# Performance work log

Hardware: AMD Instinct MI355X
Metric: run time of the kernel (lower is better)

Reference implementation:

```python
import math
import jax, jax.numpy as jnp
import numpy as np

EMBED = 512
HEADS = 2
HEAD_DIM = EMBED // HEADS


def setup_inputs() -> dict:
    key = jax.random.key(0)
    ks = jax.random.split(key, 10)
    s = 1.0 / math.sqrt(EMBED)
    return {
        "text_embeds": jax.random.normal(ks[0], (64, 32, EMBED), jnp.float32),
        "video_embeds": jax.random.normal(ks[1], (128, 64, EMBED), jnp.float32),
        "Wq": jax.random.normal(ks[2], (EMBED, EMBED), jnp.float32) * s,
        "bq": jnp.zeros((EMBED,), jnp.float32),
        "Wk": jax.random.normal(ks[3], (EMBED, EMBED), jnp.float32) * s,
        "bk": jnp.zeros((EMBED,), jnp.float32),
        "Wv": jax.random.normal(ks[4], (EMBED, EMBED), jnp.float32) * s,
        "bv": jnp.zeros((EMBED,), jnp.float32),
        "Wo": jax.random.normal(ks[5], (EMBED, EMBED), jnp.float32) * s,
        "bo": jnp.zeros((EMBED,), jnp.float32),
    }


def reference(text_embeds, video_embeds, Wq, bq, Wk, bk, Wv, bv, Wo, bo):
    num_texts, num_words, _ = text_embeds.shape
    num_vids, num_frames, _ = video_embeds.shape
    # projections (torch Linear: x @ W.T + b)
    q = (text_embeds @ Wq.T + bq).reshape(num_texts, num_words, HEADS, HEAD_DIM)
    k = (video_embeds @ Wk.T + bk).reshape(num_vids, num_frames, HEADS, HEAD_DIM)
    v = (video_embeds @ Wv.T + bv).reshape(num_vids, num_frames, HEADS, HEAD_DIM)
    # 5D cross attention logits: [vids, texts, heads, frames, words]
    logits = jnp.einsum('avhd,bthd->abhvt', k, q) / math.sqrt(HEAD_DIM)
    weights = jax.nn.softmax(logits, axis=3)  # softmax over frames
    attn = jnp.einsum('avhd,abhvt->abhtd', v, weights)  # [a,b,h,t,d]
    # faithful to torch: reshape (a,b,h,t,d) -> (a,b,t,h*d) in row-major order
    attn = attn.reshape(num_vids, num_texts, num_words, EMBED)
    attn = attn.mean(axis=0)  # [texts, words, embed]
    return attn @ Wo.T + bo
```

## Files before the change

kernel.cpp:

```cpp
#include <hip/hip_runtime.h>
#include <hip/hip_bf16.h>
#include <math.h>

#define EMBED  512
#define HEADS  2
#define HDIM   256
#define NTEXT  64
#define NWORD  32
#define NVID   128
#define NFRM   64

typedef __attribute__((ext_vector_type(8))) short      short8;
typedef __attribute__((ext_vector_type(8))) unsigned short ushort8;
typedef __attribute__((ext_vector_type(4))) float      float4v;
typedef __attribute__((ext_vector_type(4))) unsigned short ushort4v;

__device__ __forceinline__ unsigned short f2bf(float x) {
    __hip_bfloat16 h = __float2bfloat16(x);
    return *(unsigned short*)&h;
}
__device__ __forceinline__ float bf2f(unsigned short u) {
    __hip_bfloat16 h = *(__hip_bfloat16*)&u;
    return __bfloat162float(h);
}

__device__ __forceinline__ void gload_lds16(unsigned short* dst, const unsigned short* src) {
#if __has_builtin(__builtin_amdgcn_global_load_lds)
    __builtin_amdgcn_global_load_lds((const __attribute__((address_space(1))) void*)src,
                                     (__attribute__((address_space(3))) void*)dst,
                                     16, 0, 0);
#else
    *(ushort8*)dst = *(const ushort8*)src;
#endif
}

__global__ __launch_bounds__(256)
void cvt5(const float* __restrict__ s0, const float* __restrict__ s1,
          const float* __restrict__ s2, const float* __restrict__ s3,
          const float* __restrict__ s4, unsigned short* __restrict__ dst) {
    const int y = blockIdx.y;
    const float* s; size_t off; int n4;
    if (y == 0)      { s = s0; off = 0;       n4 = 262144;  }
    else if (y == 1) { s = s1; off = 1048576; n4 = 1048576; }
    else if (y == 2) { s = s2; off = 5242880; n4 = 65536;   }
    else if (y == 3) { s = s3; off = 5505024; n4 = 65536;   }
    else             { s = s4; off = 5767168; n4 = 65536;   }
    unsigned short* d = dst + off;
    for (int i = blockIdx.x * 256 + threadIdx.x; i < n4; i += 512 * 256) {
        float4v f = ((const float4v*)s)[i];
        ((ushort4v*)d)[i] = (ushort4v){f2bf(f.x), f2bf(f.y), f2bf(f.z), f2bf(f.w)};
    }
}

__global__ __launch_bounds__(256)
void proj_qkv(const unsigned short* __restrict__ text, const unsigned short* __restrict__ video,
              const unsigned short* __restrict__ Wqb, const float* __restrict__ bq,
              const unsigned short* __restrict__ Wkb, const float* __restrict__ bk,
              const unsigned short* __restrict__ Wvb, const float* __restrict__ bv,
              unsigned short* __restrict__ qout,
              unsigned short* __restrict__ Kgf, unsigned short* __restrict__ Vgf) {
    const int mb = blockIdx.x, nb = blockIdx.y;
    const int bj = nb * 128;
    const unsigned short *A, *W;
    const float* bias;
    int op, arow0, abase = 0;
    if (mb < 16)      { op = 0; A = text;  W = Wqb; bias = bq; arow0 = mb * 128; }
    else if (mb < 80) { op = 1; A = video; W = Wkb; bias = bk; abase = (mb - 16) * 2; arow0 = abase * 64; }
    else              { op = 2; A = video; W = Wvb; bias = bv; abase = (mb - 80) * 2; arow0 = abase * 64; }

    __shared__ __align__(16) unsigned char smem[65536];

    const int tid = threadIdx.x;
    const int w = tid >> 6, lane = tid & 63;
    const int lm = lane & 15, qd = lane >> 4;
    const int wr = w >> 1, wc = w & 1;

    float4v acc[4][4];
    #pragma unroll
    for (int rt = 0; rt < 4; ++rt)
        #pragma unroll
        for (int ct = 0; ct < 4; ++ct) acc[rt][ct] = (float4v){0.f, 0.f, 0.f, 0.f};

    auto STAGE = [&](int buf, int k0) {
        unsigned short* AbL = (unsigned short*)(smem + buf * 32768);
        unsigned short* WbL = (unsigned short*)(smem + buf * 32768 + 16384);
        #pragma unroll
        for (int it = 0; it < 4; ++it) {
            const int s = tid + it * 256;
            const int r = s >> 3, c8 = s & 7;
            const int sc = (c8 ^ (r & 7)) * 8;
            gload_lds16(&AbL[(size_t)s * 8], &A[(size_t)(arow0 + r) * 512 + k0 + sc]);
            gload_lds16(&WbL[(size_t)s * 8], &W[(size_t)(bj    + r) * 512 + k0 + sc]);
        }
    };

    STAGE(0, 0);
    __syncthreads();
    int cur = 0;
    for (int ks = 0; ks < 8; ++ks) {
        if (ks < 7) STAGE(cur ^ 1, (ks + 1) * 64);
        const unsigned short* AbL = (const unsigned short*)(smem + cur * 32768);
        const unsigned short* WbL = (const unsigned short*)(smem + cur * 32768 + 16384);
        #pragma unroll
        for (int kq = 0; kq < 2; ++kq) {
            const int scol = (kq * 32 + qd * 8) ^ ((lm & 7) * 8);
            short8 af[4], bf[4];
            #pragma unroll
            for (int rt = 0; rt < 4; ++rt)
                af[rt] = *(const short8*)&AbL[(wr * 64 + rt * 16 + lm) * 64 + scol];
            #pragma unroll
            for (int ct = 0; ct < 4; ++ct)
                bf[ct] = *(const short8*)&WbL[(wc * 64 + ct * 16 + lm) * 64 + scol];
            #pragma unroll
            for (int rt = 0; rt < 4; ++rt)
                #pragma unroll
                for (int ct = 0; ct < 4; ++ct)
                    acc[rt][ct] = __builtin_amdgcn_mfma_f32_16x16x32_bf16(af[rt], bf[ct], acc[rt][ct], 0, 0, 0);
        }
        __syncthreads();
        cur ^= 1;
    }

    if (op == 0) {
        #pragma unroll
        for (int rt = 0; rt < 4; ++rt)
            #pragma unroll
            for (int ct = 0; ct < 4; ++ct) {
                const int c = bj + wc * 64 + ct * 16 + lm;
                const float bb = bias[c];
                #pragma unroll
                for (int reg = 0; reg < 4; ++reg) {
                    const int r = arow0 + wr * 64 + rt * 16 + qd * 4 + reg;
                    qout[(size_t)r * 512 + c] = f2bf((acc[rt][ct][reg] + bb) * 0.0625f);
                }
            }
        return;
    }

    const int a   = abase + wr;
    const int bjs = bj + wc * 64;
    const int h      = bjs >> 8;
    const int bj_rel = bjs & 255;
    unsigned short (*Eb)[72] = (unsigned short (*)[72])(smem + w * 9216);
    const size_t base = ((size_t)(h * 128 + a)) * 16384;

    if (op == 1) {
        #pragma unroll
        for (int ct = 0; ct < 4; ++ct) {
            const int dl = ct * 16 + lm;
            const float bb = bias[bjs + dl];
            #pragma unroll
            for (int rt = 0; rt < 4; ++rt)
                #pragma unroll
                for (int reg = 0; reg < 4; ++reg)
                    Eb[rt * 16 + qd * 4 + reg][dl] = f2bf(acc[rt][ct][reg] + bb);
        }
        __syncthreads();
        #pragma unroll
        for (int it = 0; it < 8; ++it) {
            const int s = lane + it * 64;
            const int ntf = s >> 7, kqr = (s >> 6) & 1, l = s & 63;
            const int v = ntf * 16 + (l & 15);
            const int dl = kqr * 32 + (l >> 4) * 8;
            ushort8 val = *(const ushort8*)&Eb[v][dl];
            *(ushort8*)&Kgf[base + ((size_t)(ntf * 8 + (bj_rel >> 5) + kqr) * 64 + l) * 8] = val;
        }
    } else {
        #pragma unroll
        for (int ct = 0; ct < 4; ++ct) {
            const int dl = ct * 16 + lm;
            const float bb = bias[bjs + dl];
            #pragma unroll
            for (int rt = 0; rt < 4; ++rt)
                #pragma unroll
                for (int reg = 0; reg < 4; ++reg)
                    Eb[dl][rt * 16 + qd * 4 + reg] = f2bf(acc[rt][ct][reg] + bb);
        }
        __syncthreads();
        #pragma unroll
        for (int it = 0; it < 8; ++it) {
            const int s = lane + it * 64;
            const int ntr = s >> 7, kqv = (s >> 6) & 1, l = s & 63;
            const int dl = ntr * 16 + (l & 15);
            const int v0 = kqv * 32 + (l >> 4) * 8;
            ushort8 val = *(const ushort8*)&Eb[dl][v0];
            *(ushort8*)&Vgf[base + ((size_t)(((bj_rel >> 4) + ntr) * 2 + kqv) * 64 + l) * 8] = val;
        }
    }
}

__global__ __launch_bounds__(512, 2)
void attn9(const unsigned short* __restrict__ Kgf,
           const unsigned short* __restrict__ Vgf,
           const unsigned short* __restrict__ q,
           unsigned short* __restrict__ partg) {
    const int c  = blockIdx.x;
    const int h  = blockIdx.y;
    const int tg = blockIdx.z;
    const int tid = threadIdx.x;
    const int w = tid >> 6, lane = tid & 63;
    const int lm = lane & 15, qd = lane >> 4;
    const int wt = w >> 1;
    const int fh = w & 1;
    const int b = tg * 4 + wt;

    __shared__ __align__(16) unsigned short Kb[2][16384];
    __shared__ __align__(16) unsigned short Vb[2][16384];
    __shared__ __align__(16) unsigned short Pf[4][2][2][512];
    __shared__ __align__(16) float Ex[4][2][2][16][2];

    short8 qf[2][8];
    #pragma unroll
    for (int mt = 0; mt < 2; ++mt)
        #pragma unroll
        for (int kq = 0; kq < 8; ++kq)
            qf[mt][kq] = *(const short8*)
                &q[((size_t)(b * 32 + mt * 16 + lm)) * 512 + h * 256 + kq * 32 + qd * 8];

    float4v pacc[2][8];
    #pragma unroll
    for (int mt = 0; mt < 2; ++mt)
        #pragma unroll
        for (int nd = 0; nd < 8; ++nd) pacc[mt][nd] = (float4v){0.f, 0.f, 0.f, 0.f};

    const size_t vb0 = (size_t)(h * 128 + c * 16) * 16384;

    #pragma unroll
    for (int i = 0; i < 4; ++i) {
        const int s = tid + i * 512;
        gload_lds16(&Kb[0][(size_t)s * 8], &Kgf[vb0 + (size_t)s * 8]);
        gload_lds16(&Vb[0][(size_t)s * 8], &Vgf[vb0 + (size_t)s * 8]);
    }
    #pragma unroll
    for (int i = 0; i < 4; ++i) {
        const int s = tid + i * 512;
        gload_lds16(&Kb[1][(size_t)s * 8], &Kgf[vb0 + 16384 + (size_t)s * 8]);
        gload_lds16(&Vb[1][(size_t)s * 8], &Vgf[vb0 + 16384 + (size_t)s * 8]);
    }
    __syncthreads();

    for (int ai = 0; ai < 16; ++ai) {
        const int cur = ai & 1;

        float4v lacc[2][2];
        #pragma unroll
        for (int nt = 0; nt < 2; ++nt)
            #pragma unroll
            for (int mt = 0; mt < 2; ++mt) lacc[nt][mt] = (float4v){0.f, 0.f, 0.f, 0.f};
        #pragma unroll
        for (int kq = 0; kq < 8; ++kq) {
            #pragma unroll
            for (int nt = 0; nt < 2; ++nt) {
                const short8 kf = *(const short8*)
                    &Kb[cur][(((fh * 2 + nt) * 8 + kq) * 64 + lane) * 8];
                lacc[nt][0] = __builtin_amdgcn_mfma_f32_16x16x32_bf16(kf, qf[0][kq], lacc[nt][0], 0, 0, 0);
                lacc[nt][1] = __builtin_amdgcn_mfma_f32_16x16x32_bf16(kf, qf[1][kq], lacc[nt][1], 0, 0, 0);
            }
        }

        float m2[2], sv[2], e[2][2][4];
        #pragma unroll
        for (int mt = 0; mt < 2; ++mt) {
            float mm = lacc[0][mt][0];
            #pragma unroll
            for (int nt = 0; nt < 2; ++nt)
                #pragma unroll
                for (int r = 0; r < 4; ++r) mm = fmaxf(mm, lacc[nt][mt][r]);
            mm = fmaxf(mm, __shfl_xor(mm, 16));
            mm = fmaxf(mm, __shfl_xor(mm, 32));
            float ss = 0.f;
            #pragma unroll
            for (int nt = 0; nt < 2; ++nt)
                #pragma unroll
                for (int r = 0; r < 4; ++r) {
                    const float ev = __expf(lacc[nt][mt][r] - mm);
                    e[mt][nt][r] = ev;
                    ss += ev;
                }
            ss += __shfl_xor(ss, 16);
            ss += __shfl_xor(ss, 32);
            m2[mt] = mm; sv[mt] = ss;
            if (qd == 0) {
                Ex[wt][fh][mt][lm][0] = mm;
                Ex[wt][fh][mt][lm][1] = ss;
            }
        }
        __syncthreads();

        #pragma unroll
        for (int mt = 0; mt < 2; ++mt) {
            const float om = Ex[wt][fh ^ 1][mt][lm][0];
            const float os = Ex[wt][fh ^ 1][mt][lm][1];
            const float M   = fmaxf(m2[mt], om);
            const float den = sv[mt] * __expf(m2[mt] - M) + os * __expf(om - M);
            const float fac = __expf(m2[mt] - M) / den;
            #pragma unroll
            for (int nt = 0; nt < 2; ++nt) {
                ushort4v pv;
                pv.x = f2bf(e[mt][nt][0] * fac);
                pv.y = f2bf(e[mt][nt][1] * fac);
                pv.z = f2bf(e[mt][nt][2] * fac);
                pv.w = f2bf(e[mt][nt][3] * fac);
                *(ushort4v*)&Pf[wt][mt][fh][(lm + 16 * (nt * 2 + (qd >> 1))) * 8 + (qd & 1) * 4] = pv;
            }
        }
        __syncthreads();

        #pragma unroll
        for (int kqv = 0; kqv < 2; ++kqv) {
            const short8 pf0 = *(const short8*)&Pf[wt][0][kqv][lane * 8];
            const short8 pf1 = *(const short8*)&Pf[wt][1][kqv][lane * 8];
            #pragma unroll
            for (int nd = 0; nd < 8; ++nd) {
                const short8 vf = *(const short8*)
                    &Vb[cur][(((fh * 8 + nd) * 2 + kqv) * 64 + lane) * 8];
                pacc[0][nd] = __builtin_amdgcn_mfma_f32_16x16x32_bf16(pf0, vf, pacc[0][nd], 0, 0, 0);
                pacc[1][nd] = __builtin_amdgcn_mfma_f32_16x16x32_bf16(pf1, vf, pacc[1][nd], 0, 0, 0);
            }
        }
        __syncthreads();

        if (ai < 14) {
            const size_t kb = vb0 + (size_t)(ai + 2) * 16384;
            #pragma unroll
            for (int i = 0; i < 4; ++i) {
                const int s = tid + i * 512;
                gload_lds16(&Kb[cur][(size_t)s * 8], &Kgf[kb + (size_t)s * 8]);
                gload_lds16(&Vb[cur][(size_t)s * 8], &Vgf[kb + (size_t)s * 8]);
            }
        }
    }

    unsigned short* part = partg + (size_t)c * 1048576;
    #pragma unroll
    for (int mt = 0; mt < 2; ++mt)
        #pragma unroll
        for (int nd = 0; nd < 8; ++nd)
            #pragma unroll
            for (int r = 0; r < 4; ++r) {
                const int t = mt * 16 + qd * 4 + r;
                const int d = fh * 128 + nd * 16 + lm;
                const int row = b * 32 + h * 16 + (t >> 1);
                const int col = (t & 1) * 256 + d;
                part[(size_t)row * 512 + col] = f2bf(pacc[mt][nd][r]);
            }
}

__global__ __launch_bounds__(256)
void reduce8(unsigned short* __restrict__ partg) {
    const size_t i = ((size_t)blockIdx.x * 256 + threadIdx.x) * 8;
    float s[8];
    #pragma unroll
    for (int j = 0; j < 8; ++j) s[j] = 0.f;
    #pragma unroll
    for (int p = 0; p < 8; ++p) {
        ushort8 u = *(const ushort8*)&partg[(size_t)p * 1048576 + i];
        #pragma unroll
        for (int j = 0; j < 8; ++j) s[j] += bf2f(u[j]);
    }
    ushort8 o;
    #pragma unroll
    for (int j = 0; j < 8; ++j) o[j] = f2bf(s[j] * 0.0078125f);
    *(ushort8*)&partg[i] = o;
}

__global__ __launch_bounds__(256)
void proj_o(const unsigned short* __restrict__ Abf, const float* __restrict__ W,
            const float* __restrict__ bias, float* __restrict__ C) {
    __shared__ __align__(16) unsigned short Ab[64][72];
    __shared__ __align__(16) unsigned short Wb[64][72];
    const int tid = threadIdx.x;
    const int bi = blockIdx.x * 64, bj = blockIdx.y * 64;
    const int w = tid >> 6, lane = tid & 63;
    const int lm = lane & 15, qd = lane >> 4;

    float4v acc[4];
    #pragma unroll
    for (int nt = 0; nt < 4; ++nt) acc[nt] = (float4v){0.f, 0.f, 0.f, 0.f};

    for (int k0 = 0; k0 < 512; k0 += 64) {
        #pragma unroll
        for (int it = 0; it < 2; ++it) {
            const int s = tid + it * 256;
            const int r = s >> 3, c8 = (s & 7) * 8;
            *(ushort8*)&Ab[r][c8] = *(const ushort8*)&Abf[(size_t)(bi + r) * 512 + k0 + c8];
        }
        #pragma unroll
        for (int it = 0; it < 4; ++it) {
            const int s = tid + it * 256;
            const int r = s >> 4, c4 = (s & 15) * 4;
            float4v fw = *(const float4v*)&W[(size_t)(bj + r) * 512 + k0 + c4];
            *(ushort4v*)&Wb[r][c4] = (ushort4v){f2bf(fw.x), f2bf(fw.y), f2bf(fw.z), f2bf(fw.w)};
        }
        __syncthreads();
        #pragma unroll
        for (int kq = 0; kq < 2; ++kq) {
            const short8 af = *(const short8*)&Ab[w * 16 + lm][kq * 32 + qd * 8];
            #pragma unroll
            for (int nt = 0; nt < 4; ++nt) {
                const short8 bf = *(const short8*)&Wb[nt * 16 + lm][kq * 32 + qd * 8];
                acc[nt] = __builtin_amdgcn_mfma_f32_16x16x32_bf16(af, bf, acc[nt], 0, 0, 0);
            }
        }
        __syncthreads();
    }
    #pragma unroll
    for (int nt = 0; nt < 4; ++nt) {
        const int cc = bj + nt * 16 + lm;
        const float bb = bias[cc];
        #pragma unroll
        for (int reg = 0; reg < 4; ++reg) {
            const int r = bi + w * 16 + qd * 4 + reg;
            C[(size_t)r * 512 + cc] = acc[nt][reg] + bb;
        }
    }
}

extern "C" void kernel_launch(void* const* d_in, const int* in_sizes, int n_in,
                              void* d_out, int out_size, void* d_ws, size_t ws_size,
                              hipStream_t stream) {
    const float* text  = (const float*)d_in[0];
    const float* video = (const float*)d_in[1];
    const float* Wq = (const float*)d_in[2];
    const float* bq = (const float*)d_in[3];
    const float* Wk = (const float*)d_in[4];
    const float* bk = (const float*)d_in[5];
    const float* Wv = (const float*)d_in[6];
    const float* bv = (const float*)d_in[7];
    const float* Wo = (const float*)d_in[8];
    const float* bo = (const float*)d_in[9];

    unsigned short* Kgf   = (unsigned short*)d_ws;
    unsigned short* Vgf   = (unsigned short*)((char*)d_ws + (8u << 20));
    unsigned short* partg = (unsigned short*)((char*)d_ws + (16u << 20));
    unsigned short* textbf  = partg;
    unsigned short* videobf = partg + 1048576;
    unsigned short* wqbf    = partg + 5242880;
    unsigned short* wkbf    = partg + 5505024;
    unsigned short* wvbf    = partg + 5767168;
    unsigned short* qbf   = (unsigned short*)d_out;
    float*          out   = (float*)d_out;

    cvt5<<<dim3(512, 5), 256, 0, stream>>>(text, video, Wq, Wk, Wv, partg);
    proj_qkv<<<dim3(144, 4), 256, 0, stream>>>(textbf, videobf, wqbf, bq, wkbf, bk,
                                               wvbf, bv, qbf, Kgf, Vgf);
    attn9<<<dim3(8, 2, 16), 512, 0, stream>>>(Kgf, Vgf, qbf, partg);
    reduce8<<<dim3(512), 256, 0, stream>>>(partg);
    proj_o<<<dim3(32, 8), 256, 0, stream>>>(partg, Wo, bo, out);
}
```

Baseline: 167.1 us.

## Fuse fp32-to-bf16 conversion into QKV projection and partial reduction into output projection

Removes the separate conversion kernel by loading fp32 inputs and weights straight into registers in the QKV projection, converting to bf16 and writing to LDS with register-staged double buffering. Also folds the eight-way partial-sum reduction into the output projection, which now uses 256-column tiles so each block reduces its A rows only once. The intent is fewer launches and less intermediate global traffic. The cost is higher register pressure, loss of the async direct-to-LDS loads, and only 64 blocks in the output projection.

Measured after the change: 218.0 us. 1.3x slower.

```diff
diff --git a/kernel.cpp b/kernel.cpp
--- a/kernel.cpp
+++ b/kernel.cpp
@@ -35,38 +35,20 @@
 }
 
 __global__ __launch_bounds__(256)
-void cvt5(const float* __restrict__ s0, const float* __restrict__ s1,
-          const float* __restrict__ s2, const float* __restrict__ s3,
-          const float* __restrict__ s4, unsigned short* __restrict__ dst) {
-    const int y = blockIdx.y;
-    const float* s; size_t off; int n4;
-    if (y == 0)      { s = s0; off = 0;       n4 = 262144;  }
-    else if (y == 1) { s = s1; off = 1048576; n4 = 1048576; }
-    else if (y == 2) { s = s2; off = 5242880; n4 = 65536;   }
-    else if (y == 3) { s = s3; off = 5505024; n4 = 65536;   }
-    else             { s = s4; off = 5767168; n4 = 65536;   }
-    unsigned short* d = dst + off;
-    for (int i = blockIdx.x * 256 + threadIdx.x; i < n4; i += 512 * 256) {
-        float4v f = ((const float4v*)s)[i];
-        ((ushort4v*)d)[i] = (ushort4v){f2bf(f.x), f2bf(f.y), f2bf(f.z), f2bf(f.w)};
-    }
-}
-
-__global__ __launch_bounds__(256)
-void proj_qkv(const unsigned short* __restrict__ text, const unsigned short* __restrict__ video,
-              const unsigned short* __restrict__ Wqb, const float* __restrict__ bq,
-              const unsigned short* __restrict__ Wkb, const float* __restrict__ bk,
-              const unsigned short* __restrict__ Wvb, const float* __restrict__ bv,
+void proj_qkv(const float* __restrict__ text, const float* __restrict__ video,
+              const float* __restrict__ Wq, const float* __restrict__ bq,
+              const float* __restrict__ Wk, const float* __restrict__ bk,
+              const float* __restrict__ Wv, const float* __restrict__ bv,
               unsigned short* __restrict__ qout,
               unsigned short* __restrict__ Kgf, unsigned short* __restrict__ Vgf) {
     const int mb = blockIdx.x, nb = blockIdx.y;
     const int bj = nb * 128;
-    const unsigned short *A, *W;
+    const float *A, *W;
     const float* bias;
     int op, arow0, abase = 0;
-    if (mb < 16)      { op = 0; A = text;  W = Wqb; bias = bq; arow0 = mb * 128; }
-    else if (mb < 80) { op = 1; A = video; W = Wkb; bias = bk; abase = (mb - 16) * 2; arow0 = abase * 64; }
-    else              { op = 2; A = video; W = Wvb; bias = bv; abase = (mb - 80) * 2; arow0 = abase * 64; }
+    if (mb < 16)      { op = 0; A = text;  W = Wq; bias = bq; arow0 = mb * 128; }
+    else if (mb < 80) { op = 1; A = video; W = Wk; bias = bk; abase = (mb - 16) * 2; arow0 = abase * 64; }
+    else              { op = 2; A = video; W = Wv; bias = bv; abase = (mb - 80) * 2; arow0 = abase * 64; }
 
     __shared__ __align__(16) unsigned char smem[65536];
 
@@ -81,26 +63,51 @@
         #pragma unroll
         for (int ct = 0; ct < 4; ++ct) acc[rt][ct] = (float4v){0.f, 0.f, 0.f, 0.f};
 
-    auto STAGE = [&](int buf, int k0) {
-        unsigned short* AbL = (unsigned short*)(smem + buf * 32768);
-        unsigned short* WbL = (unsigned short*)(smem + buf * 32768 + 16384);
+    float4v rA[8], rW[8];
+
+    auto REG_LOAD = [&](int k0) {
         #pragma unroll
         for (int it = 0; it < 4; ++it) {
             const int s = tid + it * 256;
             const int r = s >> 3, c8 = s & 7;
             const int sc = (c8 ^ (r & 7)) * 8;
-            gload_lds16(&AbL[(size_t)s * 8], &A[(size_t)(arow0 + r) * 512 + k0 + sc]);
-            gload_lds16(&WbL[(size_t)s * 8], &W[(size_t)(bj    + r) * 512 + k0 + sc]);
+            rA[it * 2 + 0] = *(const float4v*)&A[(size_t)(arow0 + r) * 512 + k0 + sc];
+            rA[it * 2 + 1] = *(const float4v*)&A[(size_t)(arow0 + r) * 512 + k0 + sc + 4];
+            rW[it * 2 + 0] = *(const float4v*)&W[(size_t)(bj    + r) * 512 + k0 + sc];
+            rW[it * 2 + 1] = *(const float4v*)&W[(size_t)(bj    + r) * 512 + k0 + sc + 4];
         }
     };
-
-    STAGE(0, 0);
+    auto WRITE = [&](int buf) {
+        unsigned short* AbL = (unsigned short*)(smem + buf * 32768);
+        unsigned short* WbL = AbL + 8192;
+        #pragma unroll
+        for (int it = 0; it < 4; ++it) {
+            const int s = tid + it * 256;
+            ushort8 va, vw;
+            #pragma unroll
+            for (int j = 0; j < 4; ++j) {
+                va[j]     = f2bf(rA[it * 2 + 0][j]);
+                va[4 + j] = f2bf(rA[it * 2 + 1][j]);
+                vw[j]     = f2bf(rW[it * 2 + 0][j]);
+                vw[4 + j] = f2bf(rW[it * 2 + 1][j]);
+            }
+            *(ushort8*)&AbL[(size_t)s * 8] = va;
+            *(ushort8*)&WbL[(size_t)s * 8] = vw;
+        }
+    };
+
+    REG_LOAD(0);
+    WRITE(0);
+    REG_LOAD(64);
     __syncthreads();
-    int cur = 0;
+
     for (int ks = 0; ks < 8; ++ks) {
-        if (ks < 7) STAGE(cur ^ 1, (ks + 1) * 64);
-        const unsigned short* AbL = (const unsigned short*)(smem + cur * 32768);
-        const unsigned short* WbL = (const unsigned short*)(smem + cur * 32768 + 16384);
+        if (ks < 7) {
+            WRITE((ks + 1) & 1);
+            if (ks < 6) REG_LOAD((ks + 2) * 64);
+        }
+        const unsigned short* AbL = (const unsigned short*)(smem + (ks & 1) * 32768);
+        const unsigned short* WbL = (const unsigned short*)(smem + (ks & 1) * 32768 + 16384);
         #pragma unroll
         for (int kq = 0; kq < 2; ++kq) {
             const int scol = (kq * 32 + qd * 8) ^ ((lm & 7) * 8);
@@ -118,7 +125,6 @@
                     acc[rt][ct] = __builtin_amdgcn_mfma_f32_16x16x32_bf16(af[rt], bf[ct], acc[rt][ct], 0, 0, 0);
         }
         __syncthreads();
-        cur ^= 1;
     }
 
     if (op == 0) {
@@ -347,49 +353,44 @@
 }
 
 __global__ __launch_bounds__(256)
-void reduce8(unsigned short* __restrict__ partg) {
-    const size_t i = ((size_t)blockIdx.x * 256 + threadIdx.x) * 8;
-    float s[8];
-    #pragma unroll
-    for (int j = 0; j < 8; ++j) s[j] = 0.f;
-    #pragma unroll
-    for (int p = 0; p < 8; ++p) {
-        ushort8 u = *(const ushort8*)&partg[(size_t)p * 1048576 + i];
-        #pragma unroll
-        for (int j = 0; j < 8; ++j) s[j] += bf2f(u[j]);
-    }
-    ushort8 o;
-    #pragma unroll
-    for (int j = 0; j < 8; ++j) o[j] = f2bf(s[j] * 0.0078125f);
-    *(ushort8*)&partg[i] = o;
-}
-
-__global__ __launch_bounds__(256)
-void proj_o(const unsigned short* __restrict__ Abf, const float* __restrict__ W,
-            const float* __restrict__ bias, float* __restrict__ C) {
+void proj_o_red(const unsigned short* __restrict__ partg, const float* __restrict__ W,
+                const float* __restrict__ bias, float* __restrict__ C) {
     __shared__ __align__(16) unsigned short Ab[64][72];
-    __shared__ __align__(16) unsigned short Wb[64][72];
+    __shared__ __align__(16) unsigned short Wb[256][72];
     const int tid = threadIdx.x;
-    const int bi = blockIdx.x * 64, bj = blockIdx.y * 64;
+    const int bi = blockIdx.x * 64, bj0 = blockIdx.y * 256;
     const int w = tid >> 6, lane = tid & 63;
     const int lm = lane & 15, qd = lane >> 4;
 
-    float4v acc[4];
-    #pragma unroll
-    for (int nt = 0; nt < 4; ++nt) acc[nt] = (float4v){0.f, 0.f, 0.f, 0.f};
+    float4v acc[16];
+    #pragma unroll
+    for (int nt = 0; nt < 16; ++nt) acc[nt] = (float4v){0.f, 0.f, 0.f, 0.f};
 
     for (int k0 = 0; k0 < 512; k0 += 64) {
         #pragma unroll
         for (int it = 0; it < 2; ++it) {
             const int s = tid + it * 256;
             const int r = s >> 3, c8 = (s & 7) * 8;
-            *(ushort8*)&Ab[r][c8] = *(const ushort8*)&Abf[(size_t)(bi + r) * 512 + k0 + c8];
-        }
-        #pragma unroll
-        for (int it = 0; it < 4; ++it) {
+            float sum[8];
+            #pragma unroll
+            for (int j = 0; j < 8; ++j) sum[j] = 0.f;
+            #pragma unroll
+            for (int p = 0; p < 8; ++p) {
+                ushort8 u = *(const ushort8*)
+                    &partg[(size_t)p * 1048576 + (size_t)(bi + r) * 512 + k0 + c8];
+                #pragma unroll
+                for (int j = 0; j < 8; ++j) sum[j] += bf2f(u[j]);
+            }
+            ushort8 o;
+            #pragma unroll
+            for (int j = 0; j < 8; ++j) o[j] = f2bf(sum[j] * 0.0078125f);
+            *(ushort8*)&Ab[r][c8] = o;
+        }
+        #pragma unroll
+        for (int it = 0; it < 16; ++it) {
             const int s = tid + it * 256;
             const int r = s >> 4, c4 = (s & 15) * 4;
-            float4v fw = *(const float4v*)&W[(size_t)(bj + r) * 512 + k0 + c4];
+            float4v fw = *(const float4v*)&W[(size_t)(bj0 + r) * 512 + k0 + c4];
             *(ushort4v*)&Wb[r][c4] = (ushort4v){f2bf(fw.x), f2bf(fw.y), f2bf(fw.z), f2bf(fw.w)};
         }
         __syncthreads();
@@ -397,7 +398,7 @@
         for (int kq = 0; kq < 2; ++kq) {
             const short8 af = *(const short8*)&Ab[w * 16 + lm][kq * 32 + qd * 8];
             #pragma unroll
-            for (int nt = 0; nt < 4; ++nt) {
+            for (int nt = 0; nt < 16; ++nt) {
                 const short8 bf = *(const short8*)&Wb[nt * 16 + lm][kq * 32 + qd * 8];
                 acc[nt] = __builtin_amdgcn_mfma_f32_16x16x32_bf16(af, bf, acc[nt], 0, 0, 0);
             }
@@ -405,8 +406,8 @@
         __syncthreads();
     }
     #pragma unroll
-    for (int nt = 0; nt < 4; ++nt) {
-        const int cc = bj + nt * 16 + lm;
+    for (int nt = 0; nt < 16; ++nt) {
+        const int cc = bj0 + nt * 16 + lm;
         const float bb = bias[cc];
         #pragma unroll
         for (int reg = 0; reg < 4; ++reg) {
@@ -433,18 +434,11 @@
     unsigned short* Kgf   = (unsigned short*)d_ws;
     unsigned short* Vgf   = (unsigned short*)((char*)d_ws + (8u << 20));
     unsigned short* partg = (unsigned short*)((char*)d_ws + (16u << 20));
-    unsigned short* textbf  = partg;
-    unsigned short* videobf = partg + 1048576;
-    unsigned short* wqbf    = partg + 5242880;
-    unsigned short* wkbf    = partg + 5505024;
-    unsigned short* wvbf    = partg + 5767168;
     unsigned short* qbf   = (unsigned short*)d_out;
     float*          out   = (float*)d_out;
 
-    cvt5<<<dim3(512, 5), 256, 0, stream>>>(text, video, Wq, Wk, Wv, partg);
-    proj_qkv<<<dim3(144, 4), 256, 0, stream>>>(textbf, videobf, wqbf, bq, wkbf, bk,
-                                               wvbf, bv, qbf, Kgf, Vgf);
+    proj_qkv<<<dim3(144, 4), 256, 0, stream>>>(text, video, Wq, bq, Wk, bk,
+                                               Wv, bv, qbf, Kgf, Vgf);
     attn9<<<dim3(8, 2, 16), 512, 0, stream>>>(Kgf, Vgf, qbf, partg);
-    reduce8<<<dim3(512), 256, 0, stream>>>(partg);
-    proj_o<<<dim3(32, 8), 256, 0, stream>>>(partg, Wo, bo, out);
-}
+    proj_o_red<<<dim3(32, 2), 256, 0, stream>>>(partg, Wo, bo, out);
+}
```
